# Optimization experiments

Hardware: AMD Instinct MI355X
Metric: run time of the kernel (lower is better)

Reference implementation:

```python
import jax, jax.numpy as jnp
import numpy as np

HEADS = 16
THETA = 10000.0


def _rope(x, pos):
    # x: [b, h, s, d_k], pos: [b, s] int
    d_k = x.shape[-1]
    inv_freq = 1.0 / (THETA ** (jnp.arange(0, d_k, 2, dtype=jnp.float32) / d_k))  # [d_k/2]
    ang = pos[..., None].astype(jnp.float32) * inv_freq                           # [b, s, d_k/2]
    cos = jnp.cos(ang)[:, None, :, :]  # [b, 1, s, d_k/2] broadcast over heads
    sin = jnp.sin(ang)[:, None, :, :]
    x_even = x[..., 0::2]
    x_odd = x[..., 1::2]
    r_even = x_even * cos - x_odd * sin
    r_odd = x_even * sin + x_odd * cos
    return jnp.stack([r_even, r_odd], axis=-1).reshape(x.shape)


def setup_inputs() -> dict:
    key = jax.random.key(0)
    ks = jax.random.split(key, 5)
    B, S, D = 4, 2048, 1024
    std = float(np.sqrt(1.0 / D))
    def w(k):
        return jnp.clip(jax.random.normal(k, (D, D), jnp.float32) * std, -3 * std, 3 * std)
    return {
        "x": jax.random.normal(ks[0], (B, S, D), jnp.float32),
        "token_positions": jnp.broadcast_to(jnp.arange(S, dtype=jnp.int32), (B, S)),
        "wq": w(ks[1]),
        "wk": w(ks[2]),
        "wv": w(ks[3]),
        "wo": w(ks[4]),
    }


def reference(x, token_positions, wq, wk, wv, wo):
    B, S, D = x.shape
    h = HEADS
    dk = D // h
    # Projections: einsum 'hd d, ... s d -> ... s hd' == x @ W.T
    def proj(w):
        return jnp.einsum('bsd,kd->bsk', x, w).reshape(B, S, h, dk).transpose(0, 2, 1, 3)
    q = _rope(proj(wq), token_positions)  # [b,h,s,dk]
    k = _rope(proj(wk), token_positions)
    v = proj(wv)
    scores = jnp.einsum('bhqd,bhkd->bhqk', q, k) / np.sqrt(dk).astype(np.float32)
    causal = jnp.tril(jnp.ones((S, S), bool))
    scores = jnp.where(causal, scores, jnp.finfo(scores.dtype).min)
    attn = jax.nn.softmax(scores, axis=-1)
    out = jnp.einsum('bhqk,bhkd->bhqd', attn, v)        # [b,h,s,dk]
    out = out.transpose(0, 2, 1, 3).reshape(B, S, D)    # [b,s,h*dk]
    return jnp.einsum('bsv,dv->bsd', out, wo)
```

## Files before the change

### kernel.cpp

```cpp
#include <hip/hip_runtime.h>
#include <hip/hip_bf16.h>
#include <stdint.h>

typedef __bf16 bf16;
typedef __bf16 bf16x4 __attribute__((ext_vector_type(4)));
typedef __bf16 bf16x8 __attribute__((ext_vector_type(8)));
typedef float f32x4 __attribute__((ext_vector_type(4)));
typedef float f32x16 __attribute__((ext_vector_type(16)));

#define GLDS16(g, l) __builtin_amdgcn_global_load_lds( \
    (const __attribute__((address_space(1))) void*)(g), \
    (__attribute__((address_space(3))) void*)(l), 16, 0, 0)

static constexpr int S = 2048;

__global__ __launch_bounds__(256) void cvt_all(const float* __restrict__ x,
                                               const float* __restrict__ wq,
                                               const float* __restrict__ wk,
                                               const float* __restrict__ wv,
                                               const float* __restrict__ wo,
                                               const int* __restrict__ tp,
                                               bf16* __restrict__ xb,
                                               bf16* __restrict__ wqkvb,
                                               bf16* __restrict__ wob,
                                               bf16* __restrict__ tabc,
                                               bf16* __restrict__ tabs) {
  const int bid = blockIdx.x;
  if (bid >= 6144) {
    int idx = (bid - 6144) * 256 + threadIdx.x;
    int row = idx >> 5, pp = idx & 31;
    float p = (float)tp[row];
    float ang = p * exp2f((float)pp * -0.4152410118609203f);
    float sn, cs;
    sincosf(ang, &sn, &cs);
    tabc[idx] = (bf16)cs;
    tabs[idx] = (bf16)sn;
    return;
  }
  const float* src;
  bf16* dst;
  int i;
  if (bid < 4096) {
    src = x; dst = xb; i = bid * 256 + threadIdx.x;
  } else {
    int w = (bid - 4096) >> 9;
    i = ((bid - 4096) & 511) * 256 + threadIdx.x;
    src = (w == 0) ? wq : (w == 1) ? wk : (w == 2) ? wv : wo;
    dst = (w == 3) ? wob : wqkvb + (size_t)w * 1048576;
  }
  const float4* p = (const float4*)src + (size_t)i * 2;
  float4 a = p[0], b = p[1];
  bf16x8 o;
  o[0] = (bf16)a.x; o[1] = (bf16)a.y; o[2] = (bf16)a.z; o[3] = (bf16)a.w;
  o[4] = (bf16)b.x; o[5] = (bf16)b.y; o[6] = (bf16)b.z; o[7] = (bf16)b.w;
  *((bf16x8*)dst + i) = o;
}

template <int MODE>
__global__ __launch_bounds__(256, 3) void gemm_k(const bf16* __restrict__ xA,
                                                 const bf16* __restrict__ wB,
                                                 const bf16* __restrict__ tabc,
                                                 const bf16* __restrict__ tabs,
                                                 bf16* __restrict__ oq,
                                                 bf16* __restrict__ ok,
                                                 bf16* __restrict__ ov,
                                                 float* __restrict__ outf) {
  constexpr int K = 1024;
  __shared__ __align__(16) char lds[49152];
  const int t = threadIdx.x, l = t & 63, wid = t >> 6;
  const int wm = wid >> 1, wn = wid & 1;
  const int bm = blockIdx.x, bn = blockIdx.y;

  int sel, tA, tB;
  const bf16 *Ap, *Bp;
  if (MODE == 0) {
    if (bn < 16) {
      sel = bn >> 3;
      tA = bm;
      tB = bn & 7;
      Ap = xA + (size_t)tA * 128 * K;
      Bp = wB + (size_t)(sel * 1024 + tB * 128) * K;
    } else {
      sel = 2;
      tA = bn - 16;
      tB = bm;
      Ap = wB + (size_t)(2048 + tA * 128) * K;
      Bp = xA + (size_t)tB * 128 * K;
    }
  } else {
    sel = 3;
    tA = bm; tB = bn;
    Ap = xA + (size_t)tA * 128 * K;
    Bp = wB + (size_t)tB * 128 * K;
  }

  const int lrow = l >> 2;
  const int csrc = ((l & 3) ^ ((l >> 3) & 3)) * 8;
  const bf16* aS = Ap + (size_t)(wid * 32 + lrow) * K + csrc;
  const bf16* bS = Bp + (size_t)(wid * 32 + lrow) * K + csrc;

  auto stage = [&](int kt, char* base) {
    GLDS16(aS + kt, base + (wid * 32) * 64);
    GLDS16(aS + (size_t)16 * K + kt, base + (wid * 32 + 16) * 64);
    GLDS16(bS + kt, base + 8192 + (wid * 32) * 64);
    GLDS16(bS + (size_t)16 * K + kt, base + 8192 + (wid * 32 + 16) * 64);
  };

  int offA[4], offB[4];
#pragma unroll
  for (int f = 0; f < 4; f++) {
    int ra = wm * 64 + f * 16 + (l & 15);
    offA[f] = ra * 64 + (((l >> 4) ^ ((ra >> 1) & 3)) * 16);
    int rb = wn * 64 + f * 16 + (l & 15);
    offB[f] = 8192 + rb * 64 + (((l >> 4) ^ ((rb >> 1) & 3)) * 16);
  }

  f32x4 acc[4][4] = {};

  char* cur = lds;
  char* nxt = lds + 16384;
  char* ovr = lds + 32768;
  stage(0, cur);
  stage(32, nxt);
#pragma unroll 1
  for (int t_ = 0; t_ < 32; ++t_) {
    if (t_ < 31) {
      asm volatile("s_waitcnt vmcnt(4)" ::: "memory");
    } else {
      asm volatile("s_waitcnt vmcnt(0)" ::: "memory");
    }
    __builtin_amdgcn_s_barrier();
    __builtin_amdgcn_sched_barrier(0);
    if (t_ + 2 < 32) stage((t_ + 2) * 32, ovr);

    bf16x8 af[4], bg[4];
#pragma unroll
    for (int f = 0; f < 4; f++) {
      af[f] = *(const bf16x8*)(cur + offA[f]);
      bg[f] = *(const bf16x8*)(cur + offB[f]);
    }
    __builtin_amdgcn_s_setprio(1);
#pragma unroll
    for (int mi = 0; mi < 4; mi++)
#pragma unroll
      for (int ni = 0; ni < 4; ni++)
        acc[mi][ni] = __builtin_amdgcn_mfma_f32_16x16x32_bf16(
            af[mi], bg[ni], acc[mi][ni], 0, 0, 0);
    __builtin_amdgcn_s_setprio(0);
    char* tmp = cur; cur = nxt; nxt = ovr; ovr = tmp;
  }

  if (MODE == 2) {
    const int rbase = tA * 128 + wm * 64 + (l >> 4) * 4;
    const int cbase = tB * 128 + wn * 64 + (l & 15);
#pragma unroll
    for (int mi = 0; mi < 4; mi++)
#pragma unroll
      for (int ni = 0; ni < 4; ni++)
#pragma unroll
        for (int r = 0; r < 4; r++)
          outf[(size_t)(rbase + mi * 16 + r) * 1024 + cbase + ni * 16] =
              acc[mi][ni][r];
    return;
  }

  __syncthreads();
#pragma unroll 1
  for (int pass = 0; pass < 2; ++pass) {
    if (wm == pass) {
#pragma unroll
      for (int mi = 0; mi < 4; mi++)
#pragma unroll
        for (int ni = 0; ni < 4; ni++)
#pragma unroll
          for (int r = 0; r < 4; r++) {
            int rloc = mi * 16 + (l >> 4) * 4 + r;
            int col = wn * 64 + ni * 16 + (l & 15);
            *(bf16*)(lds + rloc * 272 + col * 2) = (bf16)acc[mi][ni][r];
          }
    }
    __syncthreads();
#pragma unroll 2
    for (int i = 0; i < 4; ++i) {
      const int id = t + 256 * i;
      const int rloc = id >> 4, ch = id & 15;
      bf16x8 v8 = *(const bf16x8*)(lds + rloc * 272 + ch * 16);
      const int row = pass * 64 + rloc;
      if (sel < 2) {
        const int m = tA * 128 + row;
        const int g = ch & 7;
        bf16x4 tc = *(const bf16x4*)(tabc + m * 32 + g * 4);
        bf16x4 tsn = *(const bf16x4*)(tabs + m * 32 + g * 4);
        bf16x8 o;
#pragma unroll
        for (int j = 0; j < 4; j++) {
          float cs = (float)tc[j], sn = (float)tsn[j];
          float e = (float)v8[2 * j], od = (float)v8[2 * j + 1];
          o[2 * j]     = (bf16)(e * cs - od * sn);
          o[2 * j + 1] = (bf16)(e * sn + od * cs);
        }
        bf16* dst = (sel == 0) ? oq : ok;
        const int h = tB * 2 + (ch >> 3);
        size_t idx = ((size_t)((m >> 11) * 16 + h) << 17) +
                     ((size_t)(m & 2047) << 6) + g * 8;
        *(bf16x8*)(dst + idx) = o;
      } else {
        const int dd = tA * 128 + row;
        const int h = dd >> 6;
        const int s0 = tB * 128 + ch * 8;
        size_t idx = ((size_t)((s0 >> 11) * 16 + h) << 17) +
                     ((size_t)(dd & 63) << 11) + (s0 & 2047);
        *(bf16x8*)(ov + idx) = v8;
      }
    }
    __syncthreads();
  }
}

__global__ __launch_bounds__(512, 4) void attn_k(const bf16* __restrict__ q,
                                                 const bf16* __restrict__ k,
                                                 const bf16* __restrict__ vt,
                                                 bf16* __restrict__ att) {
  __shared__ bf16 Ks[2][8192];
  __shared__ bf16 Vs[2][8192];

  const int t = threadIdx.x, l = t & 63, w = t >> 6;
  const int hi2 = l >> 5, q5 = l & 31;

  const int raw = blockIdx.x;
  const int r2 = raw & 255;
  const int wg = (r2 & 7) * 32 + (r2 >> 3);
  const int bh = ((raw < 256) ? 0 : 32) + (wg >> 3);
  const int qt = (raw < 256) ? (wg & 7) : 7 - (wg & 7);

  const bf16* qb = q + (size_t)bh * S * 64;
  const bf16* kb = k + (size_t)bh * S * 64;
  const bf16* vb = vt + (size_t)bh * 64 * S;

  const int lrow = l >> 3;
  const int clog = ((l & 7) ^ (lrow & 7)) * 8;

  auto stage = [&](int st, int b) {
#pragma unroll
    for (int sub = 0; sub < 2; sub++) {
      const int nt = 2 * st + sub;
      GLDS16(kb + (size_t)(nt * 64 + w * 8 + lrow) * 64 + clog,
             &Ks[b][sub * 4096 + w * 512]);
      GLDS16(vb + (size_t)(w * 8 + lrow) * S + nt * 64 + clog,
             &Vs[b][sub * 4096 + w * 512]);
    }
  };

  const int swz = (q5 & 7) << 4;
  int kaddr[4], vaddr[8];
#pragma unroll
  for (int c = 0; c < 4; c++)
    kaddr[c] = q5 * 128 + ((32 * c + 16 * hi2) ^ swz);
#pragma unroll
  for (int m = 0; m < 8; m++)
    vaddr[m] = q5 * 128 + ((16 * m) ^ swz) + 8 * hi2;

  const int b_ = bh >> 4, h_ = bh & 15;
  const char* KsB = (const char*)&Ks[0][0];
  const char* VsB = (const char*)&Vs[0][0];

  const int wqbase = qt * 256 + w * 32;
  const int qrow = wqbase + q5;
  bf16x8 qf[4];
#pragma unroll
  for (int c = 0; c < 4; c++) {
    bf16x8 rq = *(const bf16x8*)&qb[(size_t)qrow * 64 + 16 * c + 8 * hi2];
    bf16x8 s_;
#pragma unroll
    for (int j2 = 0; j2 < 8; j2++)
      s_[j2] = (bf16)((float)rq[j2] * 0.18033688011112042f);
    qf[c] = s_;
  }

  f32x16 acc[2] = {};
  float l_r = 0.f;
  const int nst = 2 * qt + 2;
  const int qmaxw = wqbase + 31;

  stage(0, 0);
#pragma unroll 1
  for (int s = 0; s < nst; ++s) {
    if (s + 1 < nst) {
      stage(s + 1, (s + 1) & 1);
      asm volatile("s_waitcnt vmcnt(4)" ::: "memory");
    } else {
      asm volatile("s_waitcnt vmcnt(0)" ::: "memory");
    }
    __builtin_amdgcn_s_barrier();
    __builtin_amdgcn_sched_barrier(0);

    const int bo_buf = (s & 1) * 16384;
    float rs = 0.f;
#pragma unroll
    for (int sub = 0; sub < 2; sub++) {
      const int nt = 2 * s + sub;
      if (64 * nt > qmaxw) continue;
      const int bo = bo_buf + sub * 8192;
#pragma unroll
      for (int T = 0; T < 2; T++) {
        f32x16 sc = {};
        __builtin_amdgcn_s_setprio(1);
#pragma unroll
        for (int c = 0; c < 4; c++) {
          bf16x8 kf = *(const bf16x8*)(KsB + bo + T * 4096 + kaddr[c]);
          sc = __builtin_amdgcn_mfma_f32_32x32x16_bf16(kf, qf[c], sc, 0, 0, 0);
        }
        __builtin_amdgcn_s_setprio(0);

        if (64 * nt + 32 * T + 31 > wqbase) {
#pragma unroll
          for (int r = 0; r < 16; r++) {
            int kvg = 64 * nt + 32 * T + (r & 3) + 8 * (r >> 2) + 4 * hi2;
            if (kvg > qrow) sc[r] = -1e30f;
          }
        }

        bf16x8 pa0, pa1;
#pragma unroll
        for (int r = 0; r < 8; r++) {
          float p0 = __builtin_amdgcn_exp2f(sc[r]);
          float p1 = __builtin_amdgcn_exp2f(sc[8 + r]);
          rs += p0 + p1;
          pa0[r] = (bf16)p0;
          pa1[r] = (bf16)p1;
        }

        __builtin_amdgcn_s_setprio(1);
#pragma unroll
        for (int dt = 0; dt < 2; dt++) {
          bf16x4 v0 = *(const bf16x4*)(VsB + bo + dt * 4096 + vaddr[4 * T]);
          bf16x4 v1 = *(const bf16x4*)(VsB + bo + dt * 4096 + vaddr[4 * T + 1]);
          bf16x8 bv;
#pragma unroll
          for (int j2 = 0; j2 < 4; j2++) { bv[j2] = v0[j2]; bv[4 + j2] = v1[j2]; }
          acc[dt] = __builtin_amdgcn_mfma_f32_32x32x16_bf16(pa0, bv, acc[dt], 0, 0, 0);
          v0 = *(const bf16x4*)(VsB + bo + dt * 4096 + vaddr[4 * T + 2]);
          v1 = *(const bf16x4*)(VsB + bo + dt * 4096 + vaddr[4 * T + 3]);
#pragma unroll
          for (int j2 = 0; j2 < 4; j2++) { bv[j2] = v0[j2]; bv[4 + j2] = v1[j2]; }
          acc[dt] = __builtin_amdgcn_mfma_f32_32x32x16_bf16(pa1, bv, acc[dt], 0, 0, 0);
        }
        __builtin_amdgcn_s_setprio(0);
      }
    }
    rs += __shfl_xor(rs, 32);
    l_r += rs;

    asm volatile("s_waitcnt lgkmcnt(0)" ::: "memory");
    __builtin_amdgcn_sched_barrier(0);
    __builtin_amdgcn_s_barrier();
  }

  float linv = 1.f / l_r;
#pragma unroll
  for (int r = 0; r < 16; r++) {
    int rmap = (r & 3) + 8 * (r >> 2) + 4 * hi2;
    float li = __shfl(linv, rmap);
    int rowq = wqbase + rmap;
    size_t rb = ((size_t)(b_ * S + rowq) << 10) + h_ * 64 + q5;
#pragma unroll
    for (int dt = 0; dt < 2; dt++)
      att[rb + 32 * dt] = (bf16)(acc[dt][r] * li);
  }
}

extern "C" void kernel_launch(void* const* d_in, const int* in_sizes, int n_in,
                              void* d_out, int out_size, void* d_ws, size_t ws_size,
                              hipStream_t stream) {
  const float* x  = (const float*)d_in[0];
  const int* tp   = (const int*)d_in[1];
  const float* wq = (const float*)d_in[2];
  const float* wk = (const float*)d_in[3];
  const float* wv = (const float*)d_in[4];
  const float* wo = (const float*)d_in[5];
  float* out = (float*)d_out;

  char* ws = (char*)d_ws;
  const size_t TEN = 16777216;
  bf16* x_bf    = (bf16*)(ws);
  bf16* q_bf    = (bf16*)(ws + TEN);
  bf16* k_bf    = (bf16*)(ws + 2 * TEN);
  bf16* v_bf    = (bf16*)(ws + 3 * TEN);
  bf16* wqkv_bf = (bf16*)(ws + 4 * TEN);
  bf16* wo_bf   = wqkv_bf + 3 * 1048576;
  bf16* tabc    = wo_bf + 1048576;
  bf16* tabs    = tabc + 262144;
  bf16* att_bf  = x_bf;

  cvt_all<<<7168, 256, 0, stream>>>(x, wq, wk, wv, wo, tp, x_bf, wqkv_bf,
                                    wo_bf, tabc, tabs);

  dim3 gq(64, 24);
  gemm_k<0><<<gq, 256, 0, stream>>>(x_bf, wqkv_bf, tabc, tabs, q_bf, k_bf,
                                    v_bf, nullptr);

  attn_k<<<512, 512, 0, stream>>>(q_bf, k_bf, v_bf, att_bf);

  dim3 go(64, 8);
  gemm_k<2><<<go, 256, 0, stream>>>(att_bf, wo_bf, nullptr, nullptr, nullptr,
                                    nullptr, nullptr, out);
}
```

Measured before the change: 147.9 us.

## Load GEMM B fragments directly from global into registers, shrink LDS to double buffer

The GEMM mainloop no longer stages the B tile through LDS. Each wave loads its B fragments straight from global memory into registers, double-buffered in a register ping-pong, while only A goes through LDS, now with two buffers instead of three. LDS use drops from 48 KB to 17 KB, which may allow more resident blocks and removes the LDS traffic for B. In exchange, B rows are read redundantly across the two wm waves, the global reads are less coalesced, and the stricter vmcnt(0) wait each iteration reduces prefetch depth.

```diff
diff --git a/kernel.cpp b/kernel.cpp
--- a/kernel.cpp
+++ b/kernel.cpp
@@ -66,7 +66,7 @@
                                                  bf16* __restrict__ ov,
                                                  float* __restrict__ outf) {
   constexpr int K = 1024;
-  __shared__ __align__(16) char lds[49152];
+  __shared__ __align__(16) char lds[17408];
   const int t = threadIdx.x, l = t & 63, wid = t >> 6;
   const int wm = wid >> 1, wn = wid & 1;
   const int bm = blockIdx.x, bn = blockIdx.y;
@@ -97,47 +97,46 @@
   const int lrow = l >> 2;
   const int csrc = ((l & 3) ^ ((l >> 3) & 3)) * 8;
   const bf16* aS = Ap + (size_t)(wid * 32 + lrow) * K + csrc;
-  const bf16* bS = Bp + (size_t)(wid * 32 + lrow) * K + csrc;
 
   auto stage = [&](int kt, char* base) {
     GLDS16(aS + kt, base + (wid * 32) * 64);
     GLDS16(aS + (size_t)16 * K + kt, base + (wid * 32 + 16) * 64);
-    GLDS16(bS + kt, base + 8192 + (wid * 32) * 64);
-    GLDS16(bS + (size_t)16 * K + kt, base + 8192 + (wid * 32 + 16) * 64);
   };
 
-  int offA[4], offB[4];
+  int offA[4];
 #pragma unroll
   for (int f = 0; f < 4; f++) {
     int ra = wm * 64 + f * 16 + (l & 15);
     offA[f] = ra * 64 + (((l >> 4) ^ ((ra >> 1) & 3)) * 16);
-    int rb = wn * 64 + f * 16 + (l & 15);
-    offB[f] = 8192 + rb * 64 + (((l >> 4) ^ ((rb >> 1) & 3)) * 16);
-  }
+  }
+
+  const bf16* bp[4];
+#pragma unroll
+  for (int f = 0; f < 4; f++)
+    bp[f] = Bp + (size_t)(wn * 64 + f * 16 + (l & 15)) * K + (l >> 4) * 8;
 
   f32x4 acc[4][4] = {};
-
-  char* cur = lds;
-  char* nxt = lds + 16384;
-  char* ovr = lds + 32768;
-  stage(0, cur);
-  stage(32, nxt);
-#pragma unroll 1
-  for (int t_ = 0; t_ < 32; ++t_) {
-    if (t_ < 31) {
-      asm volatile("s_waitcnt vmcnt(4)" ::: "memory");
-    } else {
-      asm volatile("s_waitcnt vmcnt(0)" ::: "memory");
-    }
+  bf16x8 bgA[4], bgB[4];
+
+  char* b0 = lds;
+  char* b1 = lds + 8192;
+
+  stage(0, b0);
+#pragma unroll
+  for (int f = 0; f < 4; f++) bgA[f] = *(const bf16x8*)(bp[f]);
+
+  auto kbody = [&](const char* curb, char* stb, int knext,
+                   bf16x8 (&bgu)[4], bf16x8 (&bgl)[4]) {
+    asm volatile("s_waitcnt vmcnt(0)" ::: "memory");
     __builtin_amdgcn_s_barrier();
     __builtin_amdgcn_sched_barrier(0);
-    if (t_ + 2 < 32) stage((t_ + 2) * 32, ovr);
-
-    bf16x8 af[4], bg[4];
-#pragma unroll
-    for (int f = 0; f < 4; f++) {
-      af[f] = *(const bf16x8*)(cur + offA[f]);
-      bg[f] = *(const bf16x8*)(cur + offB[f]);
+    if (knext < K) stage(knext, stb);
+    bf16x8 af[4];
+#pragma unroll
+    for (int f = 0; f < 4; f++) af[f] = *(const bf16x8*)(curb + offA[f]);
+    if (knext < K) {
+#pragma unroll
+      for (int f = 0; f < 4; f++) bgl[f] = *(const bf16x8*)(bp[f] + knext);
     }
     __builtin_amdgcn_s_setprio(1);
 #pragma unroll
@@ -145,9 +144,14 @@
 #pragma unroll
       for (int ni = 0; ni < 4; ni++)
         acc[mi][ni] = __builtin_amdgcn_mfma_f32_16x16x32_bf16(
-            af[mi], bg[ni], acc[mi][ni], 0, 0, 0);
+            af[mi], bgu[ni], acc[mi][ni], 0, 0, 0);
     __builtin_amdgcn_s_setprio(0);
-    char* tmp = cur; cur = nxt; nxt = ovr; ovr = tmp;
+  };
+
+#pragma unroll 1
+  for (int t2 = 0; t2 < 16; ++t2) {
+    kbody(b0, b1, (2 * t2 + 1) * 32, bgA, bgB);
+    kbody(b1, b0, (2 * t2 + 2) * 32, bgB, bgA);
   }
 
   if (MODE == 2) {
```

New measurement: 209.6 us. 1.42x slower.
